# Optimization experiments

Hardware: AMD Instinct MI355X
Metric: run time of the kernel (lower is better)

The kernel has to match this reference:

```python
import jax, jax.numpy as jnp
import numpy as np

D_MODEL = 1024
N_HEAD = 16
HEAD_DIM = D_MODEL // N_HEAD
D_FF = 4096
EPS_PROJ = 1e-8
EPS_LN = 1e-5


def _uhg_linear(x, w, b):
    """F.linear followed by projection onto the unit sphere (project_to_uhg)."""
    out = x @ w.T + b
    norm = jnp.linalg.norm(out, axis=-1, keepdims=True)
    return out / (norm + EPS_PROJ)


def _uhg_layernorm(x, weight, bias):
    # torch var(unbiased=True) -> ddof=1
    mean = x.mean(axis=-1, keepdims=True)
    d = x.shape[-1]
    var = ((x - mean) ** 2).sum(axis=-1, keepdims=True) / (d - 1)
    return (x - mean) / jnp.sqrt(var + EPS_LN) * weight + bias


def _uhg_distance_scores(q, k):
    """UHG (projective/Wildberger) distance between all (query_i, key_j) pairs.
    quadrance(a,b) = 1 - <a,b>^2 / (<a,a><b,b>);  distance = sqrt(quadrance).
    q, k: (S, H, B, hd). Returns scores = -distance, shape (S, H, B, S)."""
    dots = jnp.einsum('ihbd,jhbd->ihbj', q, k)              # (S,H,B,S)
    qn = jnp.sum(q * q, axis=-1)                            # (S,H,B)
    kn = jnp.sum(k * k, axis=-1)                            # (S,H,B)
    denom = qn[:, :, :, None] * kn.transpose(1, 2, 0)[None] + EPS_PROJ
    quad = jnp.clip(1.0 - dots * dots / denom, 0.0, None)
    return -jnp.sqrt(quad)


def _forward(src, wq, bq, wk, bk, wv, bv, wo, bo, w1, b1, w2, b2, g1, beta1, g2, beta2):
    S, B, _ = src.shape
    q = _uhg_linear(src, wq, bq)
    k = _uhg_linear(src, wk, bk)
    v = _uhg_linear(src, wv, bv)
    # (S,B,H,hd) -> (S,H,B,hd), matching the torch permute(0,2,1,3)
    q = q.reshape(S, B, N_HEAD, HEAD_DIM).transpose(0, 2, 1, 3)
    k = k.reshape(S, B, N_HEAD, HEAD_DIM).transpose(0, 2, 1, 3)
    v = v.reshape(S, B, N_HEAD, HEAD_DIM).transpose(0, 2, 1, 3)

    scores = _uhg_distance_scores(q, k)                     # (S,H,B,S)
    attn = jax.nn.softmax(scores, axis=-1)
    out = jnp.einsum('ihbj,jhbd->ihbd', attn, v)            # (S,H,B,hd)
    out = out.transpose(0, 2, 1, 3).reshape(S, B, D_MODEL)
    attn_out = _uhg_linear(out, wo, bo)

    x = _uhg_layernorm(src + attn_out, g1, beta1)
    h = jax.nn.relu(_uhg_linear(x, w1, b1))
    ff = _uhg_linear(h, w2, b2)
    x = _uhg_layernorm(x + ff, g2, beta2)
    x = x / jnp.linalg.norm(x, axis=-1, keepdims=True)
    return x


def setup_inputs() -> dict:
    key = jax.random.key(0)
    ks = jax.random.split(key, 16)
    S, B = 2048, 2
    scale_d = 1.0 / np.sqrt(D_MODEL)
    scale_ff = 1.0 / np.sqrt(D_FF)
    inp = {
        'src': jax.random.normal(ks[0], (S, B, D_MODEL), dtype=jnp.float32),
        'wq': jax.random.normal(ks[1], (D_MODEL, D_MODEL), dtype=jnp.float32) * scale_d,
        'bq': jax.random.normal(ks[2], (D_MODEL,), dtype=jnp.float32) * scale_d,
        'wk': jax.random.normal(ks[3], (D_MODEL, D_MODEL), dtype=jnp.float32) * scale_d,
        'bk': jax.random.normal(ks[4], (D_MODEL,), dtype=jnp.float32) * scale_d,
        'wv': jax.random.normal(ks[5], (D_MODEL, D_MODEL), dtype=jnp.float32) * scale_d,
        'bv': jax.random.normal(ks[6], (D_MODEL,), dtype=jnp.float32) * scale_d,
        'wo': jax.random.normal(ks[7], (D_MODEL, D_MODEL), dtype=jnp.float32) * scale_d,
        'bo': jax.random.normal(ks[8], (D_MODEL,), dtype=jnp.float32) * scale_d,
        'w1': jax.random.normal(ks[9], (D_FF, D_MODEL), dtype=jnp.float32) * scale_d,
        'b1': jax.random.normal(ks[10], (D_FF,), dtype=jnp.float32) * scale_d,
        'w2': jax.random.normal(ks[11], (D_MODEL, D_FF), dtype=jnp.float32) * scale_ff,
        'b2': jax.random.normal(ks[12], (D_MODEL,), dtype=jnp.float32) * scale_ff,
        'g1': jnp.ones((D_MODEL,), dtype=jnp.float32),
        'beta1': jnp.zeros((D_MODEL,), dtype=jnp.float32),
        'g2': jnp.ones((D_MODEL,), dtype=jnp.float32),
        'beta2': jnp.zeros((D_MODEL,), dtype=jnp.float32),
    }
    return inp


def reference(src, wq, bq, wk, bk, wv, bv, wo, bo, w1, b1, w2, b2, g1, beta1, g2, beta2):
    return _forward(src, wq, bq, wk, bk, wv, bv, wo, bo, w1, b1, w2, b2, g1, beta1, g2, beta2)
```

## Files before the change

### kernel.cpp

```cpp
#include <hip/hip_runtime.h>
#include <math.h>

#define D_MODEL 1024
#define N_HEADS 16
#define HDIM    64
#define D_FF    4096
#define SEQ     2048
#define BATCH   2
#define NTOK    (SEQ*BATCH)

typedef __attribute__((ext_vector_type(8))) short short8;
typedef __attribute__((ext_vector_type(4))) float f32x4;
typedef __attribute__((ext_vector_type(4))) unsigned short us4;

__device__ __forceinline__ unsigned short f2bf(float f) {
    union { float f; unsigned u; } x; x.f = f;
    unsigned r = x.u + 0x7fffu + ((x.u >> 16) & 1u);
    return (unsigned short)(r >> 16);
}
__device__ __forceinline__ float bf2f(unsigned short u) {
    union { unsigned u; float f; } x; x.u = ((unsigned)u) << 16; return x.f;
}

typedef __attribute__((address_space(1))) const unsigned short g_u16;
typedef __attribute__((address_space(3))) unsigned short l_u16;
__device__ __forceinline__ void gload_lds16(const unsigned short* g, unsigned short* l) {
    __builtin_amdgcn_global_load_lds((g_u16*)g, (l_u16*)l, 16, 0, 0);
}

__device__ __forceinline__ float block_sum_256(float v, volatile float* red) {
#pragma unroll
    for (int off = 32; off >= 1; off >>= 1) v += __shfl_xor(v, off, 64);
    int wid = threadIdx.x >> 6;
    __syncthreads();
    if ((threadIdx.x & 63) == 0) red[wid] = v;
    __syncthreads();
    return red[0] + red[1] + red[2] + red[3];
}

__global__ __launch_bounds__(256) void convert_bf16_kernel(
    const float* __restrict__ in, unsigned short* __restrict__ out, int n4)
{
    int i = blockIdx.x * 256 + threadIdx.x;
    if (i >= n4) return;
    float4 v = *(const float4*)&in[(size_t)i * 4];
    us4 o = { f2bf(v.x), f2bf(v.y), f2bf(v.z), f2bf(v.w) };
    *(us4*)&out[(size_t)i * 4] = o;
}

__global__ __launch_bounds__(256) void gemm_bf16_kernel(
    const unsigned short* __restrict__ A,
    const unsigned short* __restrict__ W,
    const float* __restrict__ bias,
    float* __restrict__ Y,
    int M, int K, int lda)
{
    __shared__ unsigned short As[128 * 32];
    __shared__ unsigned short Bs[128 * 32];

    const int t    = threadIdx.x;
    const int lane = t & 63;
    const int w    = t >> 6;
    const int wr   = w >> 1, wc = w & 1;
    const int i0   = blockIdx.y * 128;
    const int j0   = blockIdx.x * 128;
    const int lrow = lane & 15;
    const int lk   = (lane >> 4) * 8;

    f32x4 zero4 = {0.f, 0.f, 0.f, 0.f};
    f32x4 acc[4][4];
#pragma unroll
    for (int mi = 0; mi < 4; ++mi)
#pragma unroll
        for (int ni = 0; ni < 4; ++ni) acc[mi][ni] = zero4;

    for (int k0 = 0; k0 < K; k0 += 32) {
#pragma unroll
        for (int s = 0; s < 2; ++s) {
            int u     = s * 4 + w;
            int chunk = u * 64 + lane;
            int row   = chunk >> 2;
            int kc    = (chunk & 3) * 8;
            gload_lds16(&A[(size_t)(i0 + row) * lda + k0 + kc], &As[u * 512]);
            gload_lds16(&W[(size_t)(j0 + row) * (size_t)K + k0 + kc], &Bs[u * 512]);
        }
        __syncthreads();

        short8 af[4], bf[4];
#pragma unroll
        for (int mi = 0; mi < 4; ++mi)
            af[mi] = *(const short8*)&As[(wr * 64 + mi * 16 + lrow) * 32 + lk];
#pragma unroll
        for (int ni = 0; ni < 4; ++ni)
            bf[ni] = *(const short8*)&Bs[(wc * 64 + ni * 16 + lrow) * 32 + lk];
#pragma unroll
        for (int mi = 0; mi < 4; ++mi)
#pragma unroll
            for (int ni = 0; ni < 4; ++ni)
                acc[mi][ni] = __builtin_amdgcn_mfma_f32_16x16x32_bf16(
                    af[mi], bf[ni], acc[mi][ni], 0, 0, 0);
        __syncthreads();
    }

    const int orow = (lane >> 4) * 4;
    const int ocol = lane & 15;
#pragma unroll
    for (int ni = 0; ni < 4; ++ni) {
        int c = j0 + wc * 64 + ni * 16 + ocol;
        float bv = bias[c];
#pragma unroll
        for (int mi = 0; mi < 4; ++mi) {
            int rbase = i0 + wr * 64 + mi * 16 + orow;
#pragma unroll
            for (int r = 0; r < 4; ++r)
                Y[(size_t)(rbase + r) * M + c] = acc[mi][ni][r] + bv;
        }
    }
}

template<int M, bool RELU, bool BF16OUT>
__global__ __launch_bounds__(256) void rownorm_kernel(float* __restrict__ Y)
{
    __shared__ float red[4];
    const int row = blockIdx.x;
    const int t = threadIdx.x;
    constexpr int NV = M / 1024;
    const size_t base = (size_t)row * M;
    float4 vv[NV];
    float ss = 0.f;
#pragma unroll
    for (int u = 0; u < NV; ++u) {
        vv[u] = *(const float4*)&Y[base + (size_t)(u * 256 + t) * 4];
        ss += vv[u].x*vv[u].x + vv[u].y*vv[u].y + vv[u].z*vv[u].z + vv[u].w*vv[u].w;
    }
    ss = block_sum_256(ss, red);
    float sc = 1.f / (sqrtf(ss) + 1e-8f);
#pragma unroll
    for (int u = 0; u < NV; ++u) {
        float4 o;
        o.x = vv[u].x * sc; o.y = vv[u].y * sc;
        o.z = vv[u].z * sc; o.w = vv[u].w * sc;
        if (RELU) {
            o.x = fmaxf(o.x, 0.f); o.y = fmaxf(o.y, 0.f);
            o.z = fmaxf(o.z, 0.f); o.w = fmaxf(o.w, 0.f);
        }
        if (BF16OUT) {
            unsigned short* yb = (unsigned short*)&Y[base];
            us4 ob = { f2bf(o.x), f2bf(o.y), f2bf(o.z), f2bf(o.w) };
            *(us4*)&yb[(size_t)(u * 256 + t) * 4] = ob;
        } else {
            *(float4*)&Y[base + (size_t)(u * 256 + t) * 4] = o;
        }
    }
}

__global__ __launch_bounds__(256) void attn_mfma_kernel(
    const unsigned short* __restrict__ q,
    const unsigned short* __restrict__ k,
    const unsigned short* __restrict__ v,
    unsigned short* __restrict__ out)
{
    __shared__ unsigned short Qs[128 * 72];
    __shared__ unsigned short Ks[64 * 72];
    __shared__ unsigned short Vt[64 * 72];
    __shared__ unsigned short Ps[4][32 * 72];
    __shared__ float qn_s[128];
    __shared__ float kn_s[64];

    const int h = blockIdx.y, b = blockIdx.z;
    const int iq0 = blockIdx.x * 128;
    const int t = threadIdx.x;
    const int lane = t & 63;
    const int w = t >> 6;
    const int lrow = lane & 15;
    const int lk = (lane >> 4) * 8;
    const int g = lane >> 4;
    const int c = lane & 15;
    const int cb = h * HDIM;

    {
        const int rl = t >> 3, ch = (t & 7) * 8;
#pragma unroll
        for (int p = 0; p < 4; ++p) {
            int row = p * 32 + rl;
            size_t ga = (size_t)((iq0 + row) * BATCH + b) * 2048 + cb + ch;
            *(short8*)&Qs[row * 72 + ch] = *(const short8*)&q[ga];
        }
    }
    __syncthreads();
    {
        const int row = t >> 1, half = (t & 1) * 32;
        float s = 0.f;
#pragma unroll
        for (int dd = 0; dd < 32; dd += 8) {
            short8 x = *(const short8*)&Qs[row * 72 + half + dd];
#pragma unroll
            for (int e = 0; e < 8; ++e) {
                float f = bf2f((unsigned short)x[e]); s += f * f;
            }
        }
        s += __shfl_xor(s, 1, 64);
        if ((t & 1) == 0) qn_s[row] = s;
    }

    f32x4 zero4 = {0.f, 0.f, 0.f, 0.f};
    f32x4 acc_o[2][4];
    float m_run[2][4], l_run[2][4];
#pragma unroll
    for (int mi = 0; mi < 2; ++mi)
#pragma unroll
        for (int r = 0; r < 4; ++r) { m_run[mi][r] = -1e30f; l_run[mi][r] = 0.f; }
#pragma unroll
    for (int mi = 0; mi < 2; ++mi)
#pragma unroll
        for (int ni = 0; ni < 4; ++ni) acc_o[mi][ni] = zero4;

    for (int jt = 0; jt < SEQ / 64; ++jt) {
        const int jk0 = jt * 64;
        __syncthreads();
        {
            const int rl = t >> 3, ch = (t & 7) * 8;
#pragma unroll
            for (int p = 0; p < 2; ++p) {
                int row = p * 32 + rl;
                size_t ga = (size_t)((jk0 + row) * BATCH + b) * 2048 + cb + ch;
                *(short8*)&Ks[row * 72 + ch] = *(const short8*)&k[ga];
            }
        }
        {
            const int key0 = t & 31, chs = (t >> 5) * 8;
#pragma unroll
            for (int p = 0; p < 2; ++p) {
                int key = p * 32 + key0;
                size_t ga = (size_t)((jk0 + key) * BATCH + b) * 2048 + cb + chs;
                short8 x = *(const short8*)&v[ga];
#pragma unroll
                for (int e = 0; e < 8; ++e)
                    Vt[(chs + e) * 72 + key] = (unsigned short)x[e];
            }
        }
        __syncthreads();
        {
            const int row = t >> 2, qd = (t & 3) * 16;
            float s = 0.f;
#pragma unroll
            for (int dd = 0; dd < 16; dd += 8) {
                short8 x = *(const short8*)&Ks[row * 72 + qd + dd];
#pragma unroll
                for (int e = 0; e < 8; ++e) {
                    float f = bf2f((unsigned short)x[e]); s += f * f;
                }
            }
            s += __shfl_xor(s, 1, 64);
            s += __shfl_xor(s, 2, 64);
            if ((t & 3) == 0) kn_s[row] = s;
        }
        __syncthreads();

        f32x4 sc[2][4];
#pragma unroll
        for (int mi = 0; mi < 2; ++mi)
#pragma unroll
            for (int ni = 0; ni < 4; ++ni) sc[mi][ni] = zero4;
#pragma unroll
        for (int ks = 0; ks < 2; ++ks) {
            short8 aq[2], bk_[4];
#pragma unroll
            for (int mi = 0; mi < 2; ++mi)
                aq[mi] = *(const short8*)&Qs[(w * 32 + mi * 16 + lrow) * 72 + ks * 32 + lk];
#pragma unroll
            for (int ni = 0; ni < 4; ++ni)
                bk_[ni] = *(const short8*)&Ks[(ni * 16 + lrow) * 72 + ks * 32 + lk];
#pragma unroll
            for (int mi = 0; mi < 2; ++mi)
#pragma unroll
                for (int ni = 0; ni < 4; ++ni)
                    sc[mi][ni] = __builtin_amdgcn_mfma_f32_16x16x32_bf16(
                        aq[mi], bk_[ni], sc[mi][ni], 0, 0, 0);
        }

#pragma unroll
        for (int mi = 0; mi < 2; ++mi) {
#pragma unroll
            for (int r = 0; r < 4; ++r) {
                const int rowl = w * 32 + mi * 16 + g * 4 + r;
                const float qn_i = qn_s[rowl];
                float sv[4];
#pragma unroll
                for (int ni = 0; ni < 4; ++ni) {
                    float dot = sc[mi][ni][r];
                    float den = qn_i * kn_s[ni * 16 + c] + 1e-8f;
                    float quad = fmaxf(den - dot * dot, 0.f);
                    sv[ni] = -sqrtf(quad) * rsqrtf(den);
                }
                float tmax = fmaxf(fmaxf(sv[0], sv[1]), fmaxf(sv[2], sv[3]));
                tmax = fmaxf(tmax, __shfl_xor(tmax, 1, 16));
                tmax = fmaxf(tmax, __shfl_xor(tmax, 2, 16));
                tmax = fmaxf(tmax, __shfl_xor(tmax, 4, 16));
                tmax = fmaxf(tmax, __shfl_xor(tmax, 8, 16));
                float m_new = fmaxf(m_run[mi][r], tmax);
                float esc = __expf(m_run[mi][r] - m_new);
                float psum = 0.f;
#pragma unroll
                for (int ni = 0; ni < 4; ++ni) {
                    float p = __expf(sv[ni] - m_new);
                    Ps[w][(mi * 16 + g * 4 + r) * 72 + ni * 16 + c] = f2bf(p);
                    psum += p;
                }
                psum += __shfl_xor(psum, 1, 16);
                psum += __shfl_xor(psum, 2, 16);
                psum += __shfl_xor(psum, 4, 16);
                psum += __shfl_xor(psum, 8, 16);
                l_run[mi][r] = l_run[mi][r] * esc + psum;
                m_run[mi][r] = m_new;
#pragma unroll
                for (int ni = 0; ni < 4; ++ni) acc_o[mi][ni][r] *= esc;
            }
        }

#pragma unroll
        for (int ks = 0; ks < 2; ++ks) {
            short8 ap[2], bv_[4];
#pragma unroll
            for (int mi = 0; mi < 2; ++mi)
                ap[mi] = *(const short8*)&Ps[w][(mi * 16 + lrow) * 72 + ks * 32 + lk];
#pragma unroll
            for (int ni = 0; ni < 4; ++ni)
                bv_[ni] = *(const short8*)&Vt[(ni * 16 + lrow) * 72 + ks * 32 + lk];
#pragma unroll
            for (int mi = 0; mi < 2; ++mi)
#pragma unroll
                for (int ni = 0; ni < 4; ++ni)
                    acc_o[mi][ni] = __builtin_amdgcn_mfma_f32_16x16x32_bf16(
                        ap[mi], bv_[ni], acc_o[mi][ni], 0, 0, 0);
        }
    }

#pragma unroll
    for (int mi = 0; mi < 2; ++mi)
#pragma unroll
        for (int r = 0; r < 4; ++r) {
            float inv = 1.f / l_run[mi][r];
            int qs = iq0 + w * 32 + mi * 16 + g * 4 + r;
            size_t ob = (size_t)(qs * BATCH + b) * 1024 + cb;
#pragma unroll
            for (int ni = 0; ni < 4; ++ni)
                out[ob + ni * 16 + c] = f2bf(acc_o[mi][ni][r] * inv);
        }
}

__global__ __launch_bounds__(256) void add_ln_kernel(
    const float* __restrict__ A, const float* __restrict__ Bp,
    const float* __restrict__ g, const float* __restrict__ beta,
    float* __restrict__ Y, unsigned short* __restrict__ Yb, int finalnorm)
{
    __shared__ float red[4];
    const int row = blockIdx.x;
    const int t = threadIdx.x;
    const size_t base = (size_t)row * D_MODEL + t * 4;

    float4 a = *(const float4*)&A[base];
    float4 c = *(const float4*)&Bp[base];
    float4 vx = {a.x + c.x, a.y + c.y, a.z + c.z, a.w + c.w};

    float s = vx.x + vx.y + vx.z + vx.w;
    s = block_sum_256(s, red);
    float mean = s * (1.f / 1024.f);

    float4 dv = {vx.x - mean, vx.y - mean, vx.z - mean, vx.w - mean};
    float s2 = dv.x*dv.x + dv.y*dv.y + dv.z*dv.z + dv.w*dv.w;
    s2 = block_sum_256(s2, red);
    float rstd = rsqrtf(s2 * (1.f / 1023.f) + 1e-5f);

    float4 gg = *(const float4*)&g[t * 4];
    float4 bb = *(const float4*)&beta[t * 4];
    float4 y;
    y.x = dv.x * rstd * gg.x + bb.x;
    y.y = dv.y * rstd * gg.y + bb.y;
    y.z = dv.z * rstd * gg.z + bb.z;
    y.w = dv.w * rstd * gg.w + bb.w;

    if (finalnorm) {
        float s3 = y.x*y.x + y.y*y.y + y.z*y.z + y.w*y.w;
        s3 = block_sum_256(s3, red);
        float inv = 1.f / sqrtf(s3);
        y.x *= inv; y.y *= inv; y.z *= inv; y.w *= inv;
    }
    *(float4*)&Y[base] = y;
    if (Yb) {
        us4 ob = { f2bf(y.x), f2bf(y.y), f2bf(y.z), f2bf(y.w) };
        *(us4*)&Yb[base] = ob;
    }
}

extern "C" void kernel_launch(void* const* d_in, const int* in_sizes, int n_in,
                              void* d_out, int out_size, void* d_ws, size_t ws_size,
                              hipStream_t stream)
{
    const float* src  = (const float*)d_in[0];
    const float* wq   = (const float*)d_in[1];
    const float* bq   = (const float*)d_in[2];
    const float* wk   = (const float*)d_in[3];
    const float* bk   = (const float*)d_in[4];
    const float* wv   = (const float*)d_in[5];
    const float* bv   = (const float*)d_in[6];
    const float* wo   = (const float*)d_in[7];
    const float* bo   = (const float*)d_in[8];
    const float* w1   = (const float*)d_in[9];
    const float* b1   = (const float*)d_in[10];
    const float* w2   = (const float*)d_in[11];
    const float* b2   = (const float*)d_in[12];
    const float* g1   = (const float*)d_in[13];
    const float* be1  = (const float*)d_in[14];
    const float* g2   = (const float*)d_in[15];
    const float* be2  = (const float*)d_in[16];

    char* wsb = (char*)d_ws;
    const size_t MB = (size_t)1 << 20;
    float* qb = (float*)(wsb + 0 * MB);
    float* kb = (float*)(wsb + 16 * MB);
    float* vb = (float*)(wsb + 32 * MB);
    float* pb = (float*)(wsb + 48 * MB);
    float* xb = qb;
    float* hb = kb;
    unsigned short* srcb = (unsigned short*)(wsb + 64 * MB);
    unsigned short* abb  = (unsigned short*)(wsb + 72 * MB);
    unsigned short* wqb  = (unsigned short*)(wsb + 80 * MB);
    unsigned short* wkb  = (unsigned short*)(wsb + 82 * MB);
    unsigned short* wvb  = (unsigned short*)(wsb + 84 * MB);
    unsigned short* wob  = (unsigned short*)(wsb + 86 * MB);
    unsigned short* w1b  = (unsigned short*)(wsb + 88 * MB);
    unsigned short* w2b  = (unsigned short*)(wsb + 96 * MB);
    unsigned short* xbb  = (unsigned short*)(wsb + 104 * MB);
    unsigned short* hbb  = (unsigned short*)hb;
    unsigned short* qb16 = (unsigned short*)qb;
    unsigned short* kb16 = (unsigned short*)kb;
    unsigned short* vb16 = (unsigned short*)vb;
    float* ffb  = (float*)d_out;
    float* outp = (float*)d_out;

    dim3 blk(256);
    dim3 gP(D_MODEL / 128, NTOK / 128);
    dim3 gF(D_FF / 128, NTOK / 128);

    convert_bf16_kernel<<<(NTOK*D_MODEL/4 + 255)/256, blk, 0, stream>>>(src, srcb, NTOK*D_MODEL/4);
    convert_bf16_kernel<<<(D_MODEL*D_MODEL/4 + 255)/256, blk, 0, stream>>>(wq, wqb, D_MODEL*D_MODEL/4);
    convert_bf16_kernel<<<(D_MODEL*D_MODEL/4 + 255)/256, blk, 0, stream>>>(wk, wkb, D_MODEL*D_MODEL/4);
    convert_bf16_kernel<<<(D_MODEL*D_MODEL/4 + 255)/256, blk, 0, stream>>>(wv, wvb, D_MODEL*D_MODEL/4);
    convert_bf16_kernel<<<(D_MODEL*D_MODEL/4 + 255)/256, blk, 0, stream>>>(wo, wob, D_MODEL*D_MODEL/4);
    convert_bf16_kernel<<<(D_FF*D_MODEL/4 + 255)/256, blk, 0, stream>>>(w1, w1b, D_FF*D_MODEL/4);
    convert_bf16_kernel<<<(D_MODEL*D_FF/4 + 255)/256, blk, 0, stream>>>(w2, w2b, D_MODEL*D_FF/4);

    gemm_bf16_kernel<<<gP, blk, 0, stream>>>(srcb, wqb, bq, qb, D_MODEL, D_MODEL, D_MODEL);
    rownorm_kernel<D_MODEL, false, true><<<NTOK, blk, 0, stream>>>(qb);
    gemm_bf16_kernel<<<gP, blk, 0, stream>>>(srcb, wkb, bk, kb, D_MODEL, D_MODEL, D_MODEL);
    rownorm_kernel<D_MODEL, false, true><<<NTOK, blk, 0, stream>>>(kb);
    gemm_bf16_kernel<<<gP, blk, 0, stream>>>(srcb, wvb, bv, vb, D_MODEL, D_MODEL, D_MODEL);
    rownorm_kernel<D_MODEL, false, true><<<NTOK, blk, 0, stream>>>(vb);

    attn_mfma_kernel<<<dim3(SEQ / 128, N_HEADS, BATCH), blk, 0, stream>>>(qb16, kb16, vb16, abb);

    gemm_bf16_kernel<<<gP, blk, 0, stream>>>(abb, wob, bo, pb, D_MODEL, D_MODEL, D_MODEL);
    rownorm_kernel<D_MODEL, false, false><<<NTOK, blk, 0, stream>>>(pb);

    add_ln_kernel<<<NTOK, blk, 0, stream>>>(src, pb, g1, be1, xb, xbb, 0);

    gemm_bf16_kernel<<<gF, blk, 0, stream>>>(xbb, w1b, b1, hb, D_FF, D_MODEL, D_MODEL);
    rownorm_kernel<D_FF, true, true><<<NTOK, blk, 0, stream>>>(hb);
    gemm_bf16_kernel<<<gP, blk, 0, stream>>>(hbb, w2b, b2, ffb, D_MODEL, D_FF, 2 * D_FF);
    rownorm_kernel<D_MODEL, false, false><<<NTOK, blk, 0, stream>>>(ffb);

    add_ln_kernel<<<NTOK, blk, 0, stream>>>(xb, ffb, g2, be2, outp, nullptr, 1);
}
```

Before: 669.6 us.

## Drop online-softmax max tracking, precompute per-head norms, keep Q in registers

Scores are -sqrt(quadrance), which lies in [-1,0], so the attention kernel drops the running max, the rescaling and the per-tile shuffle reductions, and sums the exponentials only once at the end. The per-head squared norms of q and k are computed in the rownorm epilogue and read from global memory instead of being recomputed for every tile. Q fragments are held in registers rather than shared memory, the V transpose uses packed 32-bit stores, and the attention launch bounds now request 4 blocks per unit. The bounded-score assumption holds mathematically, and the norm buffers reuse workspace that is overwritten later.

New measurement: 659.7 us. No clear change (-1.5%).

```diff
diff --git a/kernel.cpp b/kernel.cpp
--- a/kernel.cpp
+++ b/kernel.cpp
@@ -119,7 +119,8 @@
 }
 
 template<int M, bool RELU, bool BF16OUT>
-__global__ __launch_bounds__(256) void rownorm_kernel(float* __restrict__ Y)
+__global__ __launch_bounds__(256) void rownorm_kernel(float* __restrict__ Y,
+                                                      float* __restrict__ hnorm)
 {
     __shared__ float red[4];
     const int row = blockIdx.x;
@@ -148,24 +149,34 @@
             unsigned short* yb = (unsigned short*)&Y[base];
             us4 ob = { f2bf(o.x), f2bf(o.y), f2bf(o.z), f2bf(o.w) };
             *(us4*)&yb[(size_t)(u * 256 + t) * 4] = ob;
+            if (M == 1024 && hnorm) {
+                float a0 = bf2f(ob.x), a1 = bf2f(ob.y);
+                float a2 = bf2f(ob.z), a3 = bf2f(ob.w);
+                float hs = a0*a0 + a1*a1 + a2*a2 + a3*a3;
+                hs += __shfl_xor(hs, 1, 16);
+                hs += __shfl_xor(hs, 2, 16);
+                hs += __shfl_xor(hs, 4, 16);
+                hs += __shfl_xor(hs, 8, 16);
+                if ((t & 15) == 0)
+                    hnorm[(t >> 4) * NTOK + (row & 1) * SEQ + (row >> 1)] = hs;
+            }
         } else {
             *(float4*)&Y[base + (size_t)(u * 256 + t) * 4] = o;
         }
     }
 }
 
-__global__ __launch_bounds__(256) void attn_mfma_kernel(
+__global__ __launch_bounds__(256, 4) void attn_mfma_kernel(
     const unsigned short* __restrict__ q,
     const unsigned short* __restrict__ k,
     const unsigned short* __restrict__ v,
+    const float* __restrict__ qn_g,
+    const float* __restrict__ kn_g,
     unsigned short* __restrict__ out)
 {
-    __shared__ unsigned short Qs[128 * 72];
     __shared__ unsigned short Ks[64 * 72];
     __shared__ unsigned short Vt[64 * 72];
     __shared__ unsigned short Ps[4][32 * 72];
-    __shared__ float qn_s[128];
-    __shared__ float kn_s[64];
 
     const int h = blockIdx.y, b = blockIdx.z;
     const int iq0 = blockIdx.x * 128;
@@ -178,42 +189,34 @@
     const int c = lane & 15;
     const int cb = h * HDIM;
 
-    {
-        const int rl = t >> 3, ch = (t & 7) * 8;
-#pragma unroll
-        for (int p = 0; p < 4; ++p) {
-            int row = p * 32 + rl;
-            size_t ga = (size_t)((iq0 + row) * BATCH + b) * 2048 + cb + ch;
-            *(short8*)&Qs[row * 72 + ch] = *(const short8*)&q[ga];
-        }
-    }
-    __syncthreads();
-    {
-        const int row = t >> 1, half = (t & 1) * 32;
-        float s = 0.f;
-#pragma unroll
-        for (int dd = 0; dd < 32; dd += 8) {
-            short8 x = *(const short8*)&Qs[row * 72 + half + dd];
-#pragma unroll
-            for (int e = 0; e < 8; ++e) {
-                float f = bf2f((unsigned short)x[e]); s += f * f;
-            }
-        }
-        s += __shfl_xor(s, 1, 64);
-        if ((t & 1) == 0) qn_s[row] = s;
-    }
+    short8 qfrag[2][2];
+#pragma unroll
+    for (int mi = 0; mi < 2; ++mi)
+#pragma unroll
+        for (int ks = 0; ks < 2; ++ks) {
+            int s = iq0 + w * 32 + mi * 16 + lrow;
+            qfrag[mi][ks] = *(const short8*)&q[(size_t)(s * BATCH + b) * 2048 + cb + ks * 32 + lk];
+        }
+    const float* qnb = qn_g + h * NTOK + b * SEQ;
+    const float* knb = kn_g + h * NTOK + b * SEQ;
+    float qn_r[2][4];
+#pragma unroll
+    for (int mi = 0; mi < 2; ++mi)
+#pragma unroll
+        for (int r = 0; r < 4; ++r)
+            qn_r[mi][r] = qnb[iq0 + w * 32 + mi * 16 + g * 4 + r];
 
     f32x4 zero4 = {0.f, 0.f, 0.f, 0.f};
     f32x4 acc_o[2][4];
-    float m_run[2][4], l_run[2][4];
+    float l_run[2][4];
 #pragma unroll
     for (int mi = 0; mi < 2; ++mi)
 #pragma unroll
-        for (int r = 0; r < 4; ++r) { m_run[mi][r] = -1e30f; l_run[mi][r] = 0.f; }
+        for (int ni = 0; ni < 4; ++ni) acc_o[mi][ni] = zero4;
 #pragma unroll
     for (int mi = 0; mi < 2; ++mi)
 #pragma unroll
-        for (int ni = 0; ni < 4; ++ni) acc_o[mi][ni] = zero4;
+        for (int r = 0; r < 4; ++r) l_run[mi][r] = 0.f;
 
     for (int jt = 0; jt < SEQ / 64; ++jt) {
         const int jk0 = jt * 64;
@@ -228,35 +231,27 @@
             }
         }
         {
-            const int key0 = t & 31, chs = (t >> 5) * 8;
+            const int kp = t & 15, dc = t >> 4;
 #pragma unroll
             for (int p = 0; p < 2; ++p) {
-                int key = p * 32 + key0;
-                size_t ga = (size_t)((jk0 + key) * BATCH + b) * 2048 + cb + chs;
-                short8 x = *(const short8*)&v[ga];
-#pragma unroll
-                for (int e = 0; e < 8; ++e)
-                    Vt[(chs + e) * 72 + key] = (unsigned short)x[e];
-            }
-        }
-        __syncthreads();
-        {
-            const int row = t >> 2, qd = (t & 3) * 16;
-            float s = 0.f;
-#pragma unroll
-            for (int dd = 0; dd < 16; dd += 8) {
-                short8 x = *(const short8*)&Ks[row * 72 + qd + dd];
-#pragma unroll
-                for (int e = 0; e < 8; ++e) {
-                    float f = bf2f((unsigned short)x[e]); s += f * f;
+                int key0 = p * 32 + kp * 2;
+                size_t ga0 = (size_t)((jk0 + key0) * BATCH + b) * 2048 + cb + dc * 4;
+                us4 v0 = *(const us4*)&v[ga0];
+                us4 v1 = *(const us4*)&v[ga0 + 2 * 2048];
+#pragma unroll
+                for (int e = 0; e < 4; ++e) {
+                    unsigned pk = (unsigned)v0[e] | ((unsigned)v1[e] << 16);
+                    *(unsigned*)&Vt[(dc * 4 + e) * 72 + p * 32 + kp * 2] = pk;
                 }
             }
-            s += __shfl_xor(s, 1, 64);
-            s += __shfl_xor(s, 2, 64);
-            if ((t & 3) == 0) kn_s[row] = s;
         }
         __syncthreads();
 
+        float kn_c[4];
+#pragma unroll
+        for (int ni = 0; ni < 4; ++ni)
+            kn_c[ni] = knb[jk0 + ni * 16 + c];
+
         f32x4 sc[2][4];
 #pragma unroll
         for (int mi = 0; mi < 2; ++mi)
@@ -264,10 +259,7 @@
             for (int ni = 0; ni < 4; ++ni) sc[mi][ni] = zero4;
 #pragma unroll
         for (int ks = 0; ks < 2; ++ks) {
-            short8 aq[2], bk_[4];
-#pragma unroll
-            for (int mi = 0; mi < 2; ++mi)
-                aq[mi] = *(const short8*)&Qs[(w * 32 + mi * 16 + lrow) * 72 + ks * 32 + lk];
+            short8 bk_[4];
 #pragma unroll
             for (int ni = 0; ni < 4; ++ni)
                 bk_[ni] = *(const short8*)&Ks[(ni * 16 + lrow) * 72 + ks * 32 + lk];
@@ -276,47 +268,25 @@
 #pragma unroll
                 for (int ni = 0; ni < 4; ++ni)
                     sc[mi][ni] = __builtin_amdgcn_mfma_f32_16x16x32_bf16(
-                        aq[mi], bk_[ni], sc[mi][ni], 0, 0, 0);
-        }
-
-#pragma unroll
-        for (int mi = 0; mi < 2; ++mi) {
+                        qfrag[mi][ks], bk_[ni], sc[mi][ni], 0, 0, 0);
+        }
+
+#pragma unroll
+        for (int mi = 0; mi < 2; ++mi)
 #pragma unroll
             for (int r = 0; r < 4; ++r) {
-                const int rowl = w * 32 + mi * 16 + g * 4 + r;
-                const float qn_i = qn_s[rowl];
-                float sv[4];
+                const float qn_i = qn_r[mi][r];
 #pragma unroll
                 for (int ni = 0; ni < 4; ++ni) {
                     float dot = sc[mi][ni][r];
-                    float den = qn_i * kn_s[ni * 16 + c] + 1e-8f;
+                    float den = qn_i * kn_c[ni] + 1e-8f;
                     float quad = fmaxf(den - dot * dot, 0.f);
-                    sv[ni] = -sqrtf(quad) * rsqrtf(den);
+                    float sv = -sqrtf(quad) * rsqrtf(den);
+                    float p = __expf(sv);
+                    l_run[mi][r] += p;
+                    Ps[w][(mi * 16 + g * 4 + r) * 72 + ni * 16 + c] = f2bf(p);
                 }
-                float tmax = fmaxf(fmaxf(sv[0], sv[1]), fmaxf(sv[2], sv[3]));
-                tmax = fmaxf(tmax, __shfl_xor(tmax, 1, 16));
-                tmax = fmaxf(tmax, __shfl_xor(tmax, 2, 16));
-                tmax = fmaxf(tmax, __shfl_xor(tmax, 4, 16));
-                tmax = fmaxf(tmax, __shfl_xor(tmax, 8, 16));
-                float m_new = fmaxf(m_run[mi][r], tmax);
-                float esc = __expf(m_run[mi][r] - m_new);
-                float psum = 0.f;
-#pragma unroll
-                for (int ni = 0; ni < 4; ++ni) {
-                    float p = __expf(sv[ni] - m_new);
-                    Ps[w][(mi * 16 + g * 4 + r) * 72 + ni * 16 + c] = f2bf(p);
-                    psum += p;
-                }
-                psum += __shfl_xor(psum, 1, 16);
-                psum += __shfl_xor(psum, 2, 16);
-                psum += __shfl_xor(psum, 4, 16);
-                psum += __shfl_xor(psum, 8, 16);
-                l_run[mi][r] = l_run[mi][r] * esc + psum;
-                m_run[mi][r] = m_new;
-#pragma unroll
-                for (int ni = 0; ni < 4; ++ni) acc_o[mi][ni][r] *= esc;
             }
-        }
 
 #pragma unroll
         for (int ks = 0; ks < 2; ++ks) {
@@ -340,7 +310,12 @@
     for (int mi = 0; mi < 2; ++mi)
 #pragma unroll
         for (int r = 0; r < 4; ++r) {
-            float inv = 1.f / l_run[mi][r];
+            float lv = l_run[mi][r];
+            lv += __shfl_xor(lv, 1, 16);
+            lv += __shfl_xor(lv, 2, 16);
+            lv += __shfl_xor(lv, 4, 16);
+            lv += __shfl_xor(lv, 8, 16);
+            float inv = 1.f / lv;
             int qs = iq0 + w * 32 + mi * 16 + g * 4 + r;
             size_t ob = (size_t)(qs * BATCH + b) * 1024 + cb;
 #pragma unroll
@@ -421,6 +396,8 @@
     float* kb = (float*)(wsb + 16 * MB);
     float* vb = (float*)(wsb + 32 * MB);
     float* pb = (float*)(wsb + 48 * MB);
+    float* qn_g = (float*)(wsb + 48 * MB);
+    float* kn_g = (float*)(wsb + 48 * MB + 256 * 1024);
     float* xb = qb;
     float* hb = kb;
     unsigned short* srcb = (unsigned short*)(wsb + 64 * MB);
@@ -452,23 +429,24 @@
     convert_bf16_kernel<<<(D_MODEL*D_FF/4 + 255)/256, blk, 0, stream>>>(w2, w2b, D_MODEL*D_FF/4);
 
     gemm_bf16_kernel<<<gP, blk, 0, stream>>>(srcb, wqb, bq, qb, D_MODEL, D_MODEL, D_MODEL);
-    rownorm_kernel<D_MODEL, false, true><<<NTOK, blk, 0, stream>>>(qb);
+    rownorm_kernel<D_MODEL, false, true><<<NTOK, blk, 0, stream>>>(qb, qn_g);
     gemm_bf16_kernel<<<gP, blk, 0, stream>>>(srcb, wkb, bk, kb, D_MODEL, D_MODEL, D_MODEL);
-    rownorm_kernel<D_MODEL, false, true><<<NTOK, blk, 0, stream>>>(kb);
+    rownorm_kernel<D_MODEL, false, true><<<NTOK, blk, 0, stream>>>(kb, kn_g);
     gemm_bf16_kernel<<<gP, blk, 0, stream>>>(srcb, wvb, bv, vb, D_MODEL, D_MODEL, D_MODEL);
-    rownorm_kernel<D_MODEL, false, true><<<NTOK, blk, 0, stream>>>(vb);
-
-    attn_mfma_kernel<<<dim3(SEQ / 128, N_HEADS, BATCH), blk, 0, stream>>>(qb16, kb16, vb16, abb);
+    rownorm_kernel<D_MODEL, false, true><<<NTOK, blk, 0, stream>>>(vb, nullptr);
+
+    attn_mfma_kernel<<<dim3(SEQ / 128, N_HEADS, BATCH), blk, 0, stream>>>(
+        qb16, kb16, vb16, qn_g, kn_g, abb);
 
     gemm_bf16_kernel<<<gP, blk, 0, stream>>>(abb, wob, bo, pb, D_MODEL, D_MODEL, D_MODEL);
-    rownorm_kernel<D_MODEL, false, false><<<NTOK, blk, 0, stream>>>(pb);
+    rownorm_kernel<D_MODEL, false, false><<<NTOK, blk, 0, stream>>>(pb, nullptr);
 
     add_ln_kernel<<<NTOK, blk, 0, stream>>>(src, pb, g1, be1, xb, xbb, 0);
 
     gemm_bf16_kernel<<<gF, blk, 0, stream>>>(xbb, w1b, b1, hb, D_FF, D_MODEL, D_MODEL);
-    rownorm_kernel<D_FF, true, true><<<NTOK, blk, 0, stream>>>(hb);
+    rownorm_kernel<D_FF, true, true><<<NTOK, blk, 0, stream>>>(hb, nullptr);
     gemm_bf16_kernel<<<gP, blk, 0, stream>>>(hbb, w2b, b2, ffb, D_MODEL, D_FF, 2 * D_FF);
-    rownorm_kernel<D_MODEL, false, false><<<NTOK, blk, 0, stream>>>(ffb);
+    rownorm_kernel<D_MODEL, false, false><<<NTOK, blk, 0, stream>>>(ffb, nullptr);
 
     add_ln_kernel<<<NTOK, blk, 0, stream>>>(xb, ffb, g2, be2, outp, nullptr, 1);
 }
```
